# Kernel tuning notes

Measured on AMD Instinct MI355X. Metric: run time of the kernel, lower is better.

The kernel has to match this reference:

```python
import jax, jax.numpy as jnp
import numpy as np

NEG = jnp.float32(-1e30)  # stand-in for -inf, safe for grads/underflow in fp32
FORBID = -100000.0        # value used in the original transitions init


def setup_inputs() -> dict:
    key = jax.random.key(0)
    k1, k2, k3, k4 = jax.random.split(key, 4)
    B, T, label_size = 512, 512, 100
    L = label_size + 2  # + START, STOP
    emit = jax.random.normal(k1, (B, T, L), jnp.float32)
    # learned transitions: small noise + forbidden-entry pattern from __init__
    trans = 0.1 * jax.random.normal(k2, (L, L), jnp.float32)
    trans = trans.at[:, L - 2].set(FORBID)  # into START
    trans = trans.at[L - 1, :].set(FORBID)  # out of STOP
    trans = trans.at[:, 0].set(FORBID)
    trans = trans.at[0, :].set(FORBID)
    # variable-length padding mask (mask[:,0] always True)
    lengths = jax.random.randint(k3, (B,), T // 2, T + 1)
    mask = jnp.arange(T)[None, :] < lengths[:, None]  # [B,T] bool
    # partial annotation mask: True = tag possible; ensure >=1 possible per pos
    um = jax.random.bernoulli(k4, 0.3, (B, T, L))
    um = um.at[:, :, 1].set(True)
    return {"emit": emit, "transitions": trans, "mask": mask,
            "uncertain_mask": um}


def _crf_nll(emit, transitions, mask, uncertain_mask):
    B, T, L = emit.shape
    START, STOP = L - 2, L - 1
    e = jnp.swapaxes(emit, 0, 1)            # [T,B,L]
    m = jnp.swapaxes(mask, 0, 1)            # [T,B]
    u = jnp.swapaxes(uncertain_mask, 0, 1)  # [T,B,L]

    # ---- partition (all paths), _get_PZ ----
    prev0 = e[0] + transitions[START][None, :]  # [B,L]

    def step(prev, inp):
        et, mt = inp
        # ns[b,i,j] = prev[b,i] + trans[i,j] + emit[t,b,j]
        ns = prev[:, :, None] + transitions[None, :, :] + et[:, None, :]
        new = jax.nn.logsumexp(ns, axis=1)
        return jnp.where(mt[:, None], new, prev), None

    prev, _ = jax.lax.scan(step, prev0, (e[1:], m[1:]))
    all_score = jax.nn.logsumexp(
        prev[:, :, None] + transitions[None, :, :], axis=1)[:, STOP].sum()

    # ---- constrained partition over possible tag sequences, _score_sentence ----
    prevg0 = jnp.where(u[0], prev0, NEG)

    def stepg(prev, inp):
        et, mt, ut = inp
        ns = prev[:, :, None] + transitions[None, :, :] + et[:, None, :]
        ns = jnp.where(ut[:, None, :], ns, NEG)  # forbid impossible tags j
        new = jax.nn.logsumexp(ns, axis=1)
        return jnp.where(mt[:, None], new, prev), None

    prevg, _ = jax.lax.scan(stepg, prevg0, (e[1:], m[1:], u[1:]))
    gold_score = jax.nn.logsumexp(
        prevg[:, :, None] + transitions[None, :, :], axis=1)[:, STOP].sum()

    return all_score - gold_score


def reference(emit, transitions, mask, uncertain_mask):
    return _crf_nll(emit, transitions, mask, uncertain_mask)
```

## Files before the change

kernel.cpp:

```cpp
#include <hip/hip_runtime.h>


typedef short s16x4 __attribute__((ext_vector_type(4)));
typedef short bf16x8 __attribute__((ext_vector_type(8)));
typedef float f32x4 __attribute__((ext_vector_type(4)));

constexpr int T = 512, L = 102;
constexpr int MS = 132;
constexpr int SLAB = 16 * MS;
constexpr int NSTEPS = 72;

__device__ __forceinline__ float bf2f(short s) {
  return __uint_as_float(((unsigned)(unsigned short)s) << 16);
}
__device__ __forceinline__ short f2bf(float x) {
  unsigned u = __float_as_uint(x);
  u += 0x7fffu + ((u >> 16) & 1u);
  return (short)(u >> 16);
}
__device__ __forceinline__ bf16x8 mk8(unsigned a, unsigned b, unsigned c,
                                      unsigned d) {
  union { unsigned u[4]; bf16x8 v; } x;
  x.u[0] = a; x.u[1] = b; x.u[2] = c; x.u[3] = d;
  return x.v;
}

#define ETILE(Tt, MM, RESv)                                                  \
  {                                                                          \
    float w0 = a[Tt][0] * bf2f(MM[0]);                                       \
    float w1 = a[Tt][1] * bf2f(MM[1]);                                       \
    float w2 = a[Tt][2] * bf2f(MM[2]);                                       \
    float w3 = a[Tt][3] * bf2f(MM[3]);                                       \
    if (RESv) { w0 *= cs; w1 *= cs; w2 *= cs; w3 *= cs; }                    \
    unsigned lo_, hi_;                                                       \
    asm("v_cvt_pk_bf16_f32 %0, %1, %2" : "=v"(lo_) : "v"(w0), "v"(w1));      \
    asm("v_cvt_pk_bf16_f32 %0, %1, %2" : "=v"(hi_) : "v"(w2), "v"(w3));      \
    pkA[Tt] = mmv ? lo_ : pkA[Tt];                                           \
    pkB[Tt] = mmv ? hi_ : pkB[Tt];                                           \
  }

#define STEP(SB, MMVv, RESv)                                                 \
  {                                                                          \
    const bool mmv = (MMVv) != 0;                                            \
    const short* sln = mlb + (SB) + cc * MS;                                 \
    const s16x4 mm0 = *(const s16x4*)(sln + 0 + 8 * hi);                     \
    const s16x4 mm1 = *(const s16x4*)(sln + 4 + 8 * hi);                     \
    const s16x4 mm2 = *(const s16x4*)(sln + 32 + 8 * hi);                    \
    const s16x4 mm3 = *(const s16x4*)(sln + 36 + 8 * hi);                    \
    const s16x4 mm4 = *(const s16x4*)(sln + 64 + 8 * hi);                    \
    const s16x4 mm5 = *(const s16x4*)(sln + 68 + 8 * hi);                    \
    const s16x4 mm6 = *(const s16x4*)(sln + 96 + 4 * hi);                    \
    const unsigned q3d0 =                                                    \
        ((unsigned)__builtin_amdgcn_ds_bpermute(bpa, (int)pkA[6])) & himask; \
    const unsigned q3d1 =                                                    \
        ((unsigned)__builtin_amdgcn_ds_bpermute(bpa, (int)pkB[6])) & himask; \
    const unsigned q3d2 =                                                    \
        ((unsigned)__builtin_amdgcn_ds_bpermute(bpb, (int)pkA[6])) & himask; \
    const unsigned q3d3 =                                                    \
        ((unsigned)__builtin_amdgcn_ds_bpermute(bpb, (int)pkB[6])) & himask; \
    const bf16x8 q0 = mk8(pkA[0], pkB[0], pkA[1], pkB[1]);                   \
    const bf16x8 q1 = mk8(pkA[2], pkB[2], pkA[3], pkB[3]);                   \
    const bf16x8 q2 = mk8(pkA[4], pkB[4], pkA[5], pkB[5]);                   \
    const bf16x8 q3 = mk8(q3d0, q3d1, q3d2, q3d3);                           \
    f32x4 a[7];                                                              \
    _Pragma("unroll") for (int Tt = 0; Tt < 7; ++Tt)                         \
      a[Tt] = __builtin_amdgcn_mfma_f32_16x16x32_bf16(ef[Tt][0], q0, zf,     \
                                                      0, 0, 0);              \
    _Pragma("unroll") for (int Tt = 0; Tt < 7; ++Tt)                         \
      a[Tt] = __builtin_amdgcn_mfma_f32_16x16x32_bf16(ef[Tt][1], q1, a[Tt],  \
                                                      0, 0, 0);              \
    _Pragma("unroll") for (int Tt = 0; Tt < 7; ++Tt)                         \
      a[Tt] = __builtin_amdgcn_mfma_f32_16x16x32_bf16(ef[Tt][2], q2, a[Tt],  \
                                                      0, 0, 0);              \
    _Pragma("unroll") for (int Tt = 0; Tt < 7; ++Tt)                         \
      a[Tt] = __builtin_amdgcn_mfma_f32_16x16x32_bf16(ef[Tt][3], q3, a[Tt],  \
                                                      0, 0, 0);              \
    float cs = 1.f;                                                          \
    if (RESv) {                                                              \
      const float w1r = a[0][1] * bf2f(mm0[1]);                              \
      const float spre = mmv ? w1r : 1.0f;                                   \
      const float sh = __shfl(spre, cc);                                     \
      cs = __builtin_amdgcn_rcpf(sh);                                        \
      logZ += __logf(sh);                                                    \
    }                                                                        \
    ETILE(0, mm0, RESv) ETILE(1, mm1, RESv) ETILE(2, mm2, RESv)              \
    ETILE(3, mm3, RESv) ETILE(4, mm4, RESv) ETILE(5, mm5, RESv)              \
    ETILE(6, mm6, RESv)                                                      \
  }

__global__ __launch_bounds__(256, 1)
void crf_scan(const float* __restrict__ emit,
              const float* __restrict__ trans,
              const unsigned char* __restrict__ mask_b,
              const unsigned char* __restrict__ um_b,
              float* __restrict__ partials)
{
  const int tid = threadIdx.x, wid = tid >> 6, lane = tid & 63;
  const int bid = blockIdx.x;
  const int grp = bid & 63, pair = bid >> 6;
  const int b8 = grp * 8;
  const int ush = (um_b[1] != 0) ? 0 : 2;

  __shared__ __align__(16) short Ml[2][8][16][MS];
  __shared__ unsigned char Kmask[8][T];
  __shared__ int sflags[4];

  volatile int* pf0 = (volatile int*)&sflags[0];
  volatile int* pf1 = (volatile int*)&sflags[1];

  if (wid >= 2) {
    const int p    = wid - 2;
    const int boff = 4 * p;
    const int tagp = 2 * lane;
    const int tagc = (tagp <= 100) ? tagp : 100;
    const bool tv  = (tagp <= 100);
    const int tf0 = (pair << 6) - 8;
    const int tf1 = ((pair + 4) << 6) - 8;

    if (lane == 0) sflags[p] = 0;
    for (int i = lane; i < 4 * T; i += 64) {
      const int bb_ = i >> 9, tt = i & 511;
      Kmask[boff + bb_][tt] =
          mask_b[(((size_t)(b8 + boff + bb_)) * T + tt) << ush];
    }

    float2 e[4][2][4];
    int u0[4][2][4], u1[4][2][4];

    auto issueG = [&](int kk) {
#pragma unroll
      for (int s = 0; s < 4; ++s) {
#pragma unroll
        for (int c2 = 0; c2 < 2; ++c2) {
          int t = (c2 ? tf1 : tf0) + kk + s;
          t = (t < 1) ? 1 : ((t > 511) ? 511 : t);
#pragma unroll
          for (int i = 0; i < 4; ++i) {
            const size_t base = ((size_t)(b8 + boff + i) * T + t) * (size_t)L;
            e[s][c2][i] = *(const float2*)(emit + base + tagc);
            if (ush == 0) {
              const unsigned us =
                  *(const unsigned short*)(um_b + base + tagc);
              u0[s][c2][i] = us & 255u; u1[s][c2][i] = us >> 8;
            } else {
              const uint2 uv = *(const uint2*)(um_b + ((base + tagc) << 2));
              u0[s][c2][i] = (int)uv.x; u1[s][c2][i] = (int)uv.y;
            }
          }
        }
      }
    };
    auto stageG = [&](int kk) {
#pragma unroll
      for (int s = 0; s < 4; ++s) {
#pragma unroll
        for (int c2 = 0; c2 < 2; ++c2) {
          short* slab = &Ml[c2][(kk + s) & 7][0][0];
#pragma unroll
          for (int i = 0; i < 4; ++i) {
            const float e0 = tv ? __expf(e[s][c2][i].x) : 0.f;
            const float e1_ = tv ? __expf(e[s][c2][i].y) : 0.f;
            const float g0 = u0[s][c2][i] ? e0 : 0.f;
            const float g1 = u1[s][c2][i] ? e1_ : 0.f;
            unsigned pe, pg;
            asm("v_cvt_pk_bf16_f32 %0, %1, %2" : "=v"(pe) : "v"(e0), "v"(e1_));
            asm("v_cvt_pk_bf16_f32 %0, %1, %2" : "=v"(pg) : "v"(g0), "v"(g1));
            *(unsigned*)(slab + (2 * (boff + i))     * MS + tagp) = pe;
            *(unsigned*)(slab + (2 * (boff + i) + 1) * MS + tagp) = pg;
          }
        }
      }
    };

    volatile int* myf = (p == 0) ? pf0 : pf1;
    volatile int* cfX = (volatile int*)&sflags[2];
    volatile int* cfY = (volatile int*)&sflags[3];
    __syncthreads();
    issueG(0);
    int csnX = 0, csnY = 0;

    for (int kk = 0; kk < NSTEPS; kk += 4) {
      if (kk >= 8) {
        const int need = kk - 4;
        if (csnX < need || csnY < need) {
          int vx, vy;
          do { vx = *cfX; vy = *cfY; } while (vx < need || vy < need);
          csnX = vx; csnY = vy;
        }
      }
      stageG(kk);
      asm volatile("s_waitcnt lgkmcnt(0)" ::: "memory");
      if (lane == 0) *myf = kk + 4;
      issueG(kk + 4);
    }
  } else {
    const int c2 = wid;
    if (lane == 0) sflags[2 + c2] = 0;
    __builtin_amdgcn_s_setprio(1);
    const int cc = lane & 15, hi = lane >> 4;
    const int myb = cc >> 1, batch = b8 + myb, goldc = cc & 1;
    const int t0c = (pair + 4 * c2) << 6;
    const int tfc = t0c - 8;
    const bool exact0 = (pair == 0) && (c2 == 0);
    const int sbase = c2 * 8 * SLAB;

    bf16x8 ef[7][4];
#pragma unroll
    for (int Tt = 0; Tt < 7; ++Tt) {
      const int g = (Tt < 6)
          ? (32 * (Tt >> 1) + 4 * (Tt & 1) + 8 * (cc >> 2) + (cc & 3))
          : (96 + cc);
#pragma unroll
      for (int kk = 0; kk < 4; ++kk) {
        bf16x8 v;
#pragma unroll
        for (int j = 0; j < 8; ++j) {
          const int k = 32 * kk + 8 * hi + j;
          float e = 0.f;
          if (k < L && g < L) e = __expf(trans[k * L + g]);
          v[j] = f2bf(e);
        }
        ef[Tt][kk] = v;
      }
    }

    unsigned pkA[7], pkB[7];
    const size_t e0b = (size_t)batch * T * L;
    if (exact0) {
#pragma unroll
      for (int Tt = 0; Tt < 7; ++Tt) {
        const int s0 = (Tt < 6) ? (32 * (Tt >> 1) + 4 * (Tt & 1) + 8 * hi)
                                : (96 + 4 * hi);
        float w[4];
#pragma unroll
        for (int r = 0; r < 4; ++r) {
          const int tg = s0 + r;
          float x = 0.f;
          if (tg < L) {
            x = __expf(emit[e0b + tg] + trans[100 * L + tg]);
            if (goldc && !um_b[((size_t)(e0b + tg)) << ush]) x = 0.f;
          }
          w[r] = x;
        }
        asm("v_cvt_pk_bf16_f32 %0, %1, %2" : "=v"(pkA[Tt]) : "v"(w[0]), "v"(w[1]));
        asm("v_cvt_pk_bf16_f32 %0, %1, %2" : "=v"(pkB[Tt]) : "v"(w[2]), "v"(w[3]));
      }
    } else {
      const unsigned one2 = 0x3F803F80u;
#pragma unroll
      for (int Tt = 0; Tt < 6; ++Tt) { pkA[Tt] = one2; pkB[Tt] = one2; }
      pkA[6] = (hi == 0) ? one2 : ((hi == 1) ? one2 : 0u);
      pkB[6] = (hi == 0) ? one2 : 0u;
    }

    const int bpa = (cc + 16 * ((2 * hi) & 3)) << 2;
    const int bpb = (cc + 16 * ((2 * hi + 1) & 3)) << 2;
    const unsigned himask = (hi < 2) ? 0xffffffffu : 0u;
    const short* mlb = &Ml[0][0][0][0];
    const unsigned* kmr = (const unsigned*)&Kmask[myb][0];
    const f32x4 zf = {0.f, 0.f, 0.f, 0.f};
    volatile int* cfv = (volatile int*)&sflags[2 + c2];
    float logZ = 0.f;
    int seen = 0;

    __syncthreads();

    for (int j = 0; j < 18; ++j) {
      const int k0 = 4 * j;
      if (seen < k0 + 4) {
        int v0, v1;
        do { v0 = *pf0; v1 = *pf1; } while (v0 < k0 + 4 || v1 < k0 + 4);
        seen = (v0 < v1) ? v0 : v1;
      }
      int x0 = sbase + ((k0 + 0) & 7) * SLAB;
      int x1 = sbase + ((k0 + 1) & 7) * SLAB;
      int x2 = sbase + ((k0 + 2) & 7) * SLAB;
      int x3 = sbase + ((k0 + 3) & 7) * SLAB;
      asm volatile("" : "+v"(x0), "+v"(x1), "+v"(x2), "+v"(x3) : "v"(seen));
      const int tb = tfc + k0;
      unsigned w = (tb >= 0) ? kmr[tb >> 2] : 0u;
      if (exact0 && tb == 0) w &= ~255u;
      const unsigned m0 = w & 255u, m1 = (w >> 8) & 255u;
      const unsigned m2 = (w >> 16) & 255u, m3 = w >> 24;
      STEP(x0, m0, false)
      STEP(x1, m1, false)
      STEP(x2, m2, false)
      STEP(x3, m3, true)
      asm volatile("s_waitcnt lgkmcnt(0)" ::: "memory");
      if (lane == 0) *cfv = k0 + 4;
      if (j == 1) logZ = 0.f;
    }

    float tot = 0.f;
#pragma unroll
    for (int Tt = 0; Tt < 7; ++Tt) {
      const int s0 = (Tt < 6) ? (32 * (Tt >> 1) + 4 * (Tt & 1) + 8 * hi)
                              : (96 + 4 * hi);
#pragma unroll
      for (int r = 0; r < 4; ++r) {
        const int tg = s0 + r;
        if (tg < L) {
          const unsigned pv = (r < 2) ? pkA[Tt] : pkB[Tt];
          const short bb = (short)((r & 1) ? (pv >> 16) : (pv & 0xffffu));
          tot += bf2f(bb) * __expf(trans[tg * L + 101]);
        }
      }
    }
    tot += __shfl_xor(tot, 16);
    tot += __shfl_xor(tot, 32);
    const int ae = (t0c + 64 >= T) ? 0 : (int)Kmask[myb][t0c + 64];
    const int own = (int)Kmask[myb][t0c] & (1 - ae);
    const float score = logZ + (own ? __logf(tot) : 0.f);
    float sgn = goldc ? -score : score;
    sgn += __shfl_xor(sgn, 1);
    sgn += __shfl_xor(sgn, 2);
    sgn += __shfl_xor(sgn, 4);
    sgn += __shfl_xor(sgn, 8);
    if (lane == 0) partials[2 * bid + c2] = sgn;
  }
}

__global__ void reduce_partials(const float* __restrict__ part,
                                float* __restrict__ out) {
  const int tid = threadIdx.x;
  float v = part[tid];
#pragma unroll
  for (int s = 1; s < 64; s <<= 1) v += __shfl_xor(v, s);
  __shared__ float ws[8];
  if ((tid & 63) == 0) ws[tid >> 6] = v;
  __syncthreads();
  if (tid == 0) {
    float t = 0.f;
#pragma unroll
    for (int w = 0; w < 8; ++w) t += ws[w];
    out[0] = t;
  }
}

extern "C" void kernel_launch(void* const* d_in, const int* in_sizes, int n_in,
                              void* d_out, int out_size, void* d_ws,
                              size_t ws_size, hipStream_t stream) {
  const float* emit = (const float*)d_in[0];
  const float* trn  = (const float*)d_in[1];
  const unsigned char* msk = (const unsigned char*)d_in[2];
  const unsigned char* umk = (const unsigned char*)d_in[3];
  float* out = (float*)d_out;
  float* pw  = (float*)d_ws;

  crf_scan<<<dim3(256), dim3(256), 0, stream>>>(emit, trn, msk, umk, pw);
  reduce_partials<<<dim3(1), dim3(512), 0, stream>>>(pw, out);
}
```

Before: 84.80 us.

## Split time axis into 32-step chunks with four consumer/producer wave pairs per block

Doubles the number of time chunks per batch group from 8 of 64 steps to 16 of 32 steps. Each block now runs four MFMA consumer waves and four producer waves, each producer feeding one consumer through its own flag pair, so the sequential scan per wave is shorter (10 iterations instead of 18). The cost is twice as many warm-up overlap steps relative to useful work, a larger LDS footprint, and more partials to reduce. Accuracy relies on the warm-up window still converging to the normalized state within 8 steps.

```diff
diff --git a/kernel.cpp b/kernel.cpp
--- a/kernel.cpp
+++ b/kernel.cpp
@@ -8,7 +8,7 @@
 constexpr int T = 512, L = 102;
 constexpr int MS = 132;
 constexpr int SLAB = 16 * MS;
-constexpr int NSTEPS = 72;
+constexpr int NSTEPS = 40;
 
 __device__ __forceinline__ float bf2f(short s) {
   return __uint_as_float(((unsigned)(unsigned short)s) << 16);
@@ -88,7 +88,7 @@
     ETILE(6, mm6, RESv)                                                      \
   }
 
-__global__ __launch_bounds__(256, 1)
+__global__ __launch_bounds__(512, 1)
 void crf_scan(const float* __restrict__ emit,
               const float* __restrict__ trans,
               const unsigned char* __restrict__ mask_b,
@@ -97,55 +97,46 @@
 {
   const int tid = threadIdx.x, wid = tid >> 6, lane = tid & 63;
   const int bid = blockIdx.x;
-  const int grp = bid & 63, pair = bid >> 6;
+  const int grp = bid & 63, quad = bid >> 6;
   const int b8 = grp * 8;
   const int ush = (um_b[1] != 0) ? 0 : 2;
 
-  __shared__ __align__(16) short Ml[2][8][16][MS];
+  __shared__ __align__(16) short Ml[4][8][16][MS];
   __shared__ unsigned char Kmask[8][T];
-  __shared__ int sflags[4];
-
-  volatile int* pf0 = (volatile int*)&sflags[0];
-  volatile int* pf1 = (volatile int*)&sflags[1];
-
-  if (wid >= 2) {
-    const int p    = wid - 2;
-    const int boff = 4 * p;
+  __shared__ int sflags[8];
+
+  if (wid >= 4) {
+    const int p    = wid - 4;
     const int tagp = 2 * lane;
     const int tagc = (tagp <= 100) ? tagp : 100;
     const bool tv  = (tagp <= 100);
-    const int tf0 = (pair << 6) - 8;
-    const int tf1 = ((pair + 4) << 6) - 8;
+    const int tfc  = ((quad + 4 * p) << 5) - 8;
 
     if (lane == 0) sflags[p] = 0;
-    for (int i = lane; i < 4 * T; i += 64) {
+    for (int i = lane; i < 2 * T; i += 64) {
       const int bb_ = i >> 9, tt = i & 511;
-      Kmask[boff + bb_][tt] =
-          mask_b[(((size_t)(b8 + boff + bb_)) * T + tt) << ush];
-    }
-
-    float2 e[4][2][4];
-    int u0[4][2][4], u1[4][2][4];
+      Kmask[2 * p + bb_][tt] =
+          mask_b[(((size_t)(b8 + 2 * p + bb_)) * T + tt) << ush];
+    }
+
+    float2 e[4][8];
+    int u0[4][8], u1[4][8];
 
     auto issueG = [&](int kk) {
 #pragma unroll
       for (int s = 0; s < 4; ++s) {
-#pragma unroll
-        for (int c2 = 0; c2 < 2; ++c2) {
-          int t = (c2 ? tf1 : tf0) + kk + s;
-          t = (t < 1) ? 1 : ((t > 511) ? 511 : t);
-#pragma unroll
-          for (int i = 0; i < 4; ++i) {
-            const size_t base = ((size_t)(b8 + boff + i) * T + t) * (size_t)L;
-            e[s][c2][i] = *(const float2*)(emit + base + tagc);
-            if (ush == 0) {
-              const unsigned us =
-                  *(const unsigned short*)(um_b + base + tagc);
-              u0[s][c2][i] = us & 255u; u1[s][c2][i] = us >> 8;
-            } else {
-              const uint2 uv = *(const uint2*)(um_b + ((base + tagc) << 2));
-              u0[s][c2][i] = (int)uv.x; u1[s][c2][i] = (int)uv.y;
-            }
+        int t = tfc + kk + s;
+        t = (t < 1) ? 1 : ((t > 511) ? 511 : t);
+#pragma unroll
+        for (int i = 0; i < 8; ++i) {
+          const size_t base = ((size_t)(b8 + i) * T + t) * (size_t)L;
+          e[s][i] = *(const float2*)(emit + base + tagc);
+          if (ush == 0) {
+            const unsigned us = *(const unsigned short*)(um_b + base + tagc);
+            u0[s][i] = us & 255u; u1[s][i] = us >> 8;
+          } else {
+            const uint2 uv = *(const uint2*)(um_b + ((base + tagc) << 2));
+            u0[s][i] = (int)uv.x; u1[s][i] = (int)uv.y;
           }
         }
       }
@@ -153,40 +144,32 @@
     auto stageG = [&](int kk) {
 #pragma unroll
       for (int s = 0; s < 4; ++s) {
-#pragma unroll
-        for (int c2 = 0; c2 < 2; ++c2) {
-          short* slab = &Ml[c2][(kk + s) & 7][0][0];
-#pragma unroll
-          for (int i = 0; i < 4; ++i) {
-            const float e0 = tv ? __expf(e[s][c2][i].x) : 0.f;
-            const float e1_ = tv ? __expf(e[s][c2][i].y) : 0.f;
-            const float g0 = u0[s][c2][i] ? e0 : 0.f;
-            const float g1 = u1[s][c2][i] ? e1_ : 0.f;
-            unsigned pe, pg;
-            asm("v_cvt_pk_bf16_f32 %0, %1, %2" : "=v"(pe) : "v"(e0), "v"(e1_));
-            asm("v_cvt_pk_bf16_f32 %0, %1, %2" : "=v"(pg) : "v"(g0), "v"(g1));
-            *(unsigned*)(slab + (2 * (boff + i))     * MS + tagp) = pe;
-            *(unsigned*)(slab + (2 * (boff + i) + 1) * MS + tagp) = pg;
-          }
+        short* slab = &Ml[p][(kk + s) & 7][0][0];
+#pragma unroll
+        for (int i = 0; i < 8; ++i) {
+          const float e0 = tv ? __expf(e[s][i].x) : 0.f;
+          const float e1_ = tv ? __expf(e[s][i].y) : 0.f;
+          const float g0 = u0[s][i] ? e0 : 0.f;
+          const float g1 = u1[s][i] ? e1_ : 0.f;
+          unsigned pe, pg;
+          asm("v_cvt_pk_bf16_f32 %0, %1, %2" : "=v"(pe) : "v"(e0), "v"(e1_));
+          asm("v_cvt_pk_bf16_f32 %0, %1, %2" : "=v"(pg) : "v"(g0), "v"(g1));
+          *(unsigned*)(slab + (2 * i)     * MS + tagp) = pe;
+          *(unsigned*)(slab + (2 * i + 1) * MS + tagp) = pg;
         }
       }
     };
 
-    volatile int* myf = (p == 0) ? pf0 : pf1;
-    volatile int* cfX = (volatile int*)&sflags[2];
-    volatile int* cfY = (volatile int*)&sflags[3];
+    volatile int* myf = (volatile int*)&sflags[p];
+    volatile int* cf  = (volatile int*)&sflags[4 + p];
     __syncthreads();
     issueG(0);
-    int csnX = 0, csnY = 0;
+    int csn = 0;
 
     for (int kk = 0; kk < NSTEPS; kk += 4) {
-      if (kk >= 8) {
-        const int need = kk - 4;
-        if (csnX < need || csnY < need) {
-          int vx, vy;
-          do { vx = *cfX; vy = *cfY; } while (vx < need || vy < need);
-          csnX = vx; csnY = vy;
-        }
+      if (kk >= 8 && csn < kk - 4) {
+        int v; do { v = *cf; } while (v < kk - 4);
+        csn = v;
       }
       stageG(kk);
       asm volatile("s_waitcnt lgkmcnt(0)" ::: "memory");
@@ -195,13 +178,14 @@
     }
   } else {
     const int c2 = wid;
-    if (lane == 0) sflags[2 + c2] = 0;
+    if (lane == 0) sflags[4 + c2] = 0;
     __builtin_amdgcn_s_setprio(1);
     const int cc = lane & 15, hi = lane >> 4;
     const int myb = cc >> 1, batch = b8 + myb, goldc = cc & 1;
-    const int t0c = (pair + 4 * c2) << 6;
+    const int ck  = quad + 4 * c2;
+    const int t0c = ck << 5;
     const int tfc = t0c - 8;
-    const bool exact0 = (pair == 0) && (c2 == 0);
+    const bool exact0 = (ck == 0);
     const int sbase = c2 * 8 * SLAB;
 
     bf16x8 ef[7][4];
@@ -259,18 +243,18 @@
     const short* mlb = &Ml[0][0][0][0];
     const unsigned* kmr = (const unsigned*)&Kmask[myb][0];
     const f32x4 zf = {0.f, 0.f, 0.f, 0.f};
-    volatile int* cfv = (volatile int*)&sflags[2 + c2];
+    volatile int* pfm = (volatile int*)&sflags[c2];
+    volatile int* cfv = (volatile int*)&sflags[4 + c2];
     float logZ = 0.f;
     int seen = 0;
 
     __syncthreads();
 
-    for (int j = 0; j < 18; ++j) {
+    for (int j = 0; j < 10; ++j) {
       const int k0 = 4 * j;
       if (seen < k0 + 4) {
-        int v0, v1;
-        do { v0 = *pf0; v1 = *pf1; } while (v0 < k0 + 4 || v1 < k0 + 4);
-        seen = (v0 < v1) ? v0 : v1;
+        int v; do { v = *pfm; } while (v < k0 + 4);
+        seen = v;
       }
       int x0 = sbase + ((k0 + 0) & 7) * SLAB;
       int x1 = sbase + ((k0 + 1) & 7) * SLAB;
@@ -308,7 +292,7 @@
     }
     tot += __shfl_xor(tot, 16);
     tot += __shfl_xor(tot, 32);
-    const int ae = (t0c + 64 >= T) ? 0 : (int)Kmask[myb][t0c + 64];
+    const int ae = (t0c + 32 >= T) ? 0 : (int)Kmask[myb][t0c + 32];
     const int own = (int)Kmask[myb][t0c] & (1 - ae);
     const float score = logZ + (own ? __logf(tot) : 0.f);
     float sgn = goldc ? -score : score;
@@ -316,7 +300,7 @@
     sgn += __shfl_xor(sgn, 2);
     sgn += __shfl_xor(sgn, 4);
     sgn += __shfl_xor(sgn, 8);
-    if (lane == 0) partials[2 * bid + c2] = sgn;
+    if (lane == 0) partials[4 * bid + c2] = sgn;
   }
 }
 
@@ -326,13 +310,13 @@
   float v = part[tid];
 #pragma unroll
   for (int s = 1; s < 64; s <<= 1) v += __shfl_xor(v, s);
-  __shared__ float ws[8];
+  __shared__ float ws[16];
   if ((tid & 63) == 0) ws[tid >> 6] = v;
   __syncthreads();
   if (tid == 0) {
     float t = 0.f;
 #pragma unroll
-    for (int w = 0; w < 8; ++w) t += ws[w];
+    for (int w = 0; w < 16; ++w) t += ws[w];
     out[0] = t;
   }
 }
@@ -347,6 +331,6 @@
   float* out = (float*)d_out;
   float* pw  = (float*)d_ws;
 
-  crf_scan<<<dim3(256), dim3(256), 0, stream>>>(emit, trn, msk, umk, pw);
-  reduce_partials<<<dim3(1), dim3(512), 0, stream>>>(pw, out);
-}
+  crf_scan<<<dim3(256), dim3(512), 0, stream>>>(emit, trn, msk, umk, pw);
+  reduce_partials<<<dim3(1), dim3(1024), 0, stream>>>(pw, out);
+}
```

Result: faster. 78.04 us (-8.0%).
